# Kernel optimization log

Measured on AMD Instinct MI355X. Metric: run time of the kernel, lower is better.

Reference implementation:

```python
import jax, jax.numpy as jnp
import numpy as np

NUM_EMBEDDINGS = 8192
EMBEDDING_DIM = 256
COMMITMENT_COST = 0.25


def setup_inputs() -> dict:
    key = jax.random.key(0)
    k1, k2 = jax.random.split(key)
    inputs = jax.random.normal(k1, (16, 2048, EMBEDDING_DIM), dtype=jnp.float32)
    # codebook initialized uniform(-1/K, 1/K) as in the torch module
    codebook = jax.random.uniform(
        k2, (NUM_EMBEDDINGS, EMBEDDING_DIM), dtype=jnp.float32,
        minval=-1.0 / NUM_EMBEDDINGS, maxval=1.0 / NUM_EMBEDDINGS)
    return {"inputs": inputs, "codebook": codebook}


def reference(inputs, codebook):
    B, T, D = inputs.shape
    flat = inputs.reshape(-1, D)                      # [BT, D]
    distances = (
        jnp.sum(flat * flat, axis=1, keepdims=True)
        + jnp.sum(codebook * codebook, axis=1)
        - 2.0 * jnp.matmul(flat, codebook.T)
    )
    idx = jnp.argmin(distances, axis=1)               # [BT]
    quantized = codebook[idx].reshape(B, T, D)        # gather == one-hot @ codebook
    e_latent_loss = jnp.mean((jax.lax.stop_gradient(quantized) - inputs) ** 2)
    q_latent_loss = jnp.mean((quantized - jax.lax.stop_gradient(inputs)) ** 2)
    loss = q_latent_loss + COMMITMENT_COST * e_latent_loss
    # straight-through estimator
    quantized_st = inputs + jax.lax.stop_gradient(quantized - inputs)
    return quantized_st, idx.reshape(B, T), loss
```

## Files before the change

### kernel.cpp

```cpp
#include <hip/hip_runtime.h>
#include <hip/hip_bf16.h>
#include <stdint.h>

#define D      256
#define K      8192
#define NROWS  32768
#define QELEMS 8388608

typedef __attribute__((ext_vector_type(8))) short bf16x8;
typedef __attribute__((ext_vector_type(4))) float f32x4;
typedef unsigned int u32;
typedef unsigned short u16;

__device__ __forceinline__ u16 f2bf(float f) {
    u32 b = __float_as_uint(f);
    return (u16)((b + 0x7fffu + ((b >> 16) & 1u)) >> 16);
}

__global__ __launch_bounds__(256) void vq_prep_kernel(
    const float* __restrict__ cb, u16* __restrict__ ch,
    float* __restrict__ se, float* __restrict__ loss_sum) {
    int row = blockIdx.x * 4 + (threadIdx.x >> 6);
    int l = threadIdx.x & 63;
    float4 v = *(const float4*)(cb + (size_t)row * D + l * 4);
    ushort4 o;
    o.x = f2bf(v.x); o.y = f2bf(v.y); o.z = f2bf(v.z); o.w = f2bf(v.w);
    *(ushort4*)(ch + (size_t)row * D + l * 4) = o;
    float s = v.x * v.x + v.y * v.y + v.z * v.z + v.w * v.w;
    #pragma unroll
    for (int off = 32; off > 0; off >>= 1) s += __shfl_down(s, off, 64);
    if (l == 0) se[row] = s;
    if (blockIdx.x == 0 && threadIdx.x == 0) *loss_sum = 0.f;
}

__global__ __launch_bounds__(256) void vq_filter_kernel(
    const u16* __restrict__ ch, const float* __restrict__ x,
    const float* __restrict__ se, u32* __restrict__ cand)
{
    __shared__ u16 As[2][16384];

    const int tid  = threadIdx.x;
    const int lane = tid & 63;
    const int wave = tid >> 6;
    const int m_w  = wave & 1;
    const int n_w  = wave >> 1;
    const int l15  = lane & 15;
    const int l4   = lane >> 4;
    const int row0 = blockIdx.x * 64;

    bf16x8 Bf[2][8];
    #pragma unroll
    for (int nt = 0; nt < 2; ++nt) {
        const float* xr = x + (size_t)(row0 + n_w * 32 + nt * 16 + l15) * D + l4 * 8;
        #pragma unroll
        for (int c = 0; c < 8; ++c) {
            float4 a = *(const float4*)(xr + c * 32);
            float4 b = *(const float4*)(xr + c * 32 + 4);
            bf16x8 f;
            f[0] = (short)f2bf(a.x); f[1] = (short)f2bf(a.y);
            f[2] = (short)f2bf(a.z); f[3] = (short)f2bf(a.w);
            f[4] = (short)f2bf(b.x); f[5] = (short)f2bf(b.y);
            f[6] = (short)f2bf(b.z); f[7] = (short)f2bf(b.w);
            Bf[nt][c] = f;
        }
    }

    float b0[2], b1[2]; int c0[2], c1[2];
    #pragma unroll
    for (int nt = 0; nt < 2; ++nt) { b0[nt] = 1e30f; b1[nt] = 1e30f; c0[nt] = 0; c1[nt] = 0; }

    #pragma unroll
    for (int i = 0; i < 8; ++i) {
        int g = wave * 8 + i;
        const u16* gp = ch + (size_t)((g & 3) * 16 + l15) * D + (g >> 2) * 32 + l4 * 8;
        u16* lb = &As[0][(size_t)g * 512];
        __builtin_amdgcn_global_load_lds(
            (const __attribute__((address_space(1))) u32*)gp,
            (__attribute__((address_space(3))) u32*)lb, 16, 0, 0);
    }
    __syncthreads();

    int buf = 0;
    #pragma unroll 1
    for (int ct = 0; ct < 128; ++ct) {
        const int k0 = ct << 6;

        if (ct + 1 < 128) {
            const int kn = (ct + 1) << 6;
            #pragma unroll
            for (int i = 0; i < 8; ++i) {
                int g = wave * 8 + i;
                const u16* gp = ch + (size_t)(kn + (g & 3) * 16 + l15) * D + (g >> 2) * 32 + l4 * 8;
                u16* lb = &As[buf ^ 1][(size_t)g * 512];
                __builtin_amdgcn_global_load_lds(
                    (const __attribute__((address_space(1))) u32*)gp,
                    (__attribute__((address_space(3))) u32*)lb, 16, 0, 0);
            }
        }

        const u16* cb_t = &As[buf][0];
        f32x4 acc[2][2];
        #pragma unroll
        for (int mt = 0; mt < 2; ++mt)
            #pragma unroll
            for (int nt = 0; nt < 2; ++nt) acc[mt][nt] = (f32x4){0.f, 0.f, 0.f, 0.f};

        #pragma unroll
        for (int c = 0; c < 8; ++c) {
            bf16x8 Af0 = *(const bf16x8*)(cb_t + (size_t)((c * 4 + m_w * 2 + 0) * 64 + lane) * 8);
            bf16x8 Af1 = *(const bf16x8*)(cb_t + (size_t)((c * 4 + m_w * 2 + 1) * 64 + lane) * 8);
            acc[0][0] = __builtin_amdgcn_mfma_f32_16x16x32_bf16(Af0, Bf[0][c], acc[0][0], 0, 0, 0);
            acc[0][1] = __builtin_amdgcn_mfma_f32_16x16x32_bf16(Af0, Bf[1][c], acc[0][1], 0, 0, 0);
            acc[1][0] = __builtin_amdgcn_mfma_f32_16x16x32_bf16(Af1, Bf[0][c], acc[1][0], 0, 0, 0);
            acc[1][1] = __builtin_amdgcn_mfma_f32_16x16x32_bf16(Af1, Bf[1][c], acc[1][1], 0, 0, 0);
        }

        f32x4 sev[2];
        #pragma unroll
        for (int mt = 0; mt < 2; ++mt)
            sev[mt] = *(const f32x4*)(se + k0 + (m_w * 2 + mt) * 16 + l4 * 4);

        #pragma unroll
        for (int nt = 0; nt < 2; ++nt) {
            float tmn = 1e30f;
            #pragma unroll
            for (int mt = 0; mt < 2; ++mt)
                #pragma unroll
                for (int r = 0; r < 4; ++r)
                    tmn = fminf(tmn, fmaf(-2.f, acc[mt][nt][r], sev[mt][r]));
            if (tmn < b1[nt]) {
                #pragma unroll
                for (int mt = 0; mt < 2; ++mt)
                    #pragma unroll
                    for (int r = 0; r < 4; ++r) {
                        float t = fmaf(-2.f, acc[mt][nt][r], sev[mt][r]);
                        int  cv = k0 + (m_w * 2 + mt) * 16 + l4 * 4 + r;
                        bool in0 = t < b0[nt];
                        bool in1 = t < b1[nt];
                        float ob0 = b0[nt]; int oc0 = c0[nt];
                        b1[nt] = in0 ? ob0 : (in1 ? t  : b1[nt]);
                        c1[nt] = in0 ? oc0 : (in1 ? cv : c1[nt]);
                        b0[nt] = in0 ? t  : ob0;
                        c0[nt] = in0 ? cv : oc0;
                    }
            }
        }

        __syncthreads();
        buf ^= 1;
    }

    #pragma unroll
    for (int nt = 0; nt < 2; ++nt) {
        int row = row0 + n_w * 32 + nt * 16 + l15;
        int sl  = (m_w * 4 + l4) * 2;
        cand[(size_t)row * 16 + sl]     = (u32)c0[nt];
        cand[(size_t)row * 16 + sl + 1] = (u32)c1[nt];
    }
}

__global__ __launch_bounds__(1024) void vq_rescore_kernel(
    const float* __restrict__ x, const float* __restrict__ cb,
    const float* __restrict__ se, const u32* __restrict__ cand,
    float* __restrict__ out, float* __restrict__ loss_sum)
{
    const int wave = threadIdx.x >> 6;
    const int lane = threadIdx.x & 63;
    const int row  = blockIdx.x * 16 + wave;

    float4 xv = *(const float4*)(x + (size_t)row * D + lane * 4);
    float sx = xv.x * xv.x + xv.y * xv.y + xv.z * xv.z + xv.w * xv.w;
    #pragma unroll
    for (int o = 1; o < 64; o <<= 1) sx += __shfl_xor(sx, o, 64);

    u32 myc = cand[(size_t)row * 16 + (lane & 15)];
    float best = 1e30f; int bk = 0x7fffffff;
    #pragma unroll 4
    for (int j = 0; j < 16; ++j) {
        int code = __shfl((int)myc, j, 64);
        float4 ev = *(const float4*)(cb + (size_t)code * D + lane * 4);
        float p = xv.x * ev.x + xv.y * ev.y + xv.z * ev.z + xv.w * ev.w;
        #pragma unroll
        for (int o = 1; o < 64; o <<= 1) p += __shfl_xor(p, o, 64);
        float dist = (sx + se[code]) - 2.0f * p;
        if (dist < best || (dist == best && code < bk)) { best = dist; bk = code; }
    }

    float4 q = *(const float4*)(cb + (size_t)bk * D + lane * 4);
    *(float4*)(out + (size_t)row * D + lane * 4) = q;
    float dx = q.x - xv.x, dy = q.y - xv.y, dz = q.z - xv.z, dw = q.w - xv.w;
    float s = dx * dx + dy * dy + dz * dz + dw * dw;
    #pragma unroll
    for (int o = 1; o < 64; o <<= 1) s += __shfl_xor(s, o, 64);
    if (lane == 0) out[QELEMS + row] = (float)bk;

    __shared__ float red[16];
    if (lane == 0) red[wave] = s;
    __syncthreads();
    if (threadIdx.x == 0) {
        float t = 0.f;
        #pragma unroll
        for (int w2 = 0; w2 < 16; ++w2) t += red[w2];
        atomicAdd(loss_sum, t);
    }
}

__global__ void vq_fin_kernel(const float* __restrict__ loss_sum, float* __restrict__ out) {
    out[QELEMS + NROWS] = 1.25f * (*loss_sum) * (1.0f / (float)QELEMS);
}

extern "C" void kernel_launch(void* const* d_in, const int* in_sizes, int n_in,
                              void* d_out, int out_size, void* d_ws, size_t ws_size,
                              hipStream_t stream) {
    const float* x  = (const float*)d_in[0];
    const float* cb = (const float*)d_in[1];
    float* out = (float*)d_out;

    u16* ch = (u16*)d_out;

    char* ws = (char*)d_ws;
    float* loss_sum = (float*)ws;
    float* sebuf    = (float*)(ws + 4096);
    u32*   cand     = (u32*)(ws + 65536);

    vq_prep_kernel<<<K / 4, 256, 0, stream>>>(cb, ch, sebuf, loss_sum);
    vq_filter_kernel<<<NROWS / 64, 256, 0, stream>>>(ch, x, sebuf, cand);
    vq_rescore_kernel<<<NROWS / 16, 1024, 0, stream>>>(x, cb, sebuf, cand, out, loss_sum);
    vq_fin_kernel<<<1, 1, 0, stream>>>(loss_sum, out);
}
```

Measured before the change: 393.9 us.

## Give each wave all 64 rows and one codebook slice, merge top-2 via LDS

The filter kernel's wave tiling changes so each wave holds bf16 fragments for all 64 input rows and takes a single 16-code slice of every codebook tile. Each LDS A-fragment read now feeds four MFMAs instead of two, halving LDS traffic per MFMA, and only one se vector is loaded per tile. Per-lane top-2 lists are merged pairwise through shared memory at the end so the candidate count stays at 16 per row. The cost is more registers for the input fragments and a launch_bounds occupancy hint of 2, which can force spills or limit occupancy.

```diff
diff --git a/kernel.cpp b/kernel.cpp
--- a/kernel.cpp
+++ b/kernel.cpp
@@ -33,25 +33,23 @@
     if (blockIdx.x == 0 && threadIdx.x == 0) *loss_sum = 0.f;
 }
 
-__global__ __launch_bounds__(256) void vq_filter_kernel(
+__global__ __launch_bounds__(256, 2) void vq_filter_kernel(
     const u16* __restrict__ ch, const float* __restrict__ x,
     const float* __restrict__ se, u32* __restrict__ cand)
 {
-    __shared__ u16 As[2][16384];
+    __shared__ __align__(16) u16 As[2][16384];
 
     const int tid  = threadIdx.x;
     const int lane = tid & 63;
     const int wave = tid >> 6;
-    const int m_w  = wave & 1;
-    const int n_w  = wave >> 1;
     const int l15  = lane & 15;
     const int l4   = lane >> 4;
     const int row0 = blockIdx.x * 64;
 
-    bf16x8 Bf[2][8];
-    #pragma unroll
-    for (int nt = 0; nt < 2; ++nt) {
-        const float* xr = x + (size_t)(row0 + n_w * 32 + nt * 16 + l15) * D + l4 * 8;
+    bf16x8 Bf[4][8];
+    #pragma unroll
+    for (int nt = 0; nt < 4; ++nt) {
+        const float* xr = x + (size_t)(row0 + nt * 16 + l15) * D + l4 * 8;
         #pragma unroll
         for (int c = 0; c < 8; ++c) {
             float4 a = *(const float4*)(xr + c * 32);
@@ -65,9 +63,9 @@
         }
     }
 
-    float b0[2], b1[2]; int c0[2], c1[2];
-    #pragma unroll
-    for (int nt = 0; nt < 2; ++nt) { b0[nt] = 1e30f; b1[nt] = 1e30f; c0[nt] = 0; c1[nt] = 0; }
+    float b0[4], b1[4]; int c0[4], c1[4];
+    #pragma unroll
+    for (int nt = 0; nt < 4; ++nt) { b0[nt] = 1e30f; b1[nt] = 1e30f; c0[nt] = 0; c1[nt] = 0; }
 
     #pragma unroll
     for (int i = 0; i < 8; ++i) {
@@ -99,50 +97,41 @@
         }
 
         const u16* cb_t = &As[buf][0];
-        f32x4 acc[2][2];
-        #pragma unroll
-        for (int mt = 0; mt < 2; ++mt)
-            #pragma unroll
-            for (int nt = 0; nt < 2; ++nt) acc[mt][nt] = (f32x4){0.f, 0.f, 0.f, 0.f};
+        f32x4 acc[4];
+        #pragma unroll
+        for (int nt = 0; nt < 4; ++nt) acc[nt] = (f32x4){0.f, 0.f, 0.f, 0.f};
 
         #pragma unroll
         for (int c = 0; c < 8; ++c) {
-            bf16x8 Af0 = *(const bf16x8*)(cb_t + (size_t)((c * 4 + m_w * 2 + 0) * 64 + lane) * 8);
-            bf16x8 Af1 = *(const bf16x8*)(cb_t + (size_t)((c * 4 + m_w * 2 + 1) * 64 + lane) * 8);
-            acc[0][0] = __builtin_amdgcn_mfma_f32_16x16x32_bf16(Af0, Bf[0][c], acc[0][0], 0, 0, 0);
-            acc[0][1] = __builtin_amdgcn_mfma_f32_16x16x32_bf16(Af0, Bf[1][c], acc[0][1], 0, 0, 0);
-            acc[1][0] = __builtin_amdgcn_mfma_f32_16x16x32_bf16(Af1, Bf[0][c], acc[1][0], 0, 0, 0);
-            acc[1][1] = __builtin_amdgcn_mfma_f32_16x16x32_bf16(Af1, Bf[1][c], acc[1][1], 0, 0, 0);
-        }
-
-        f32x4 sev[2];
-        #pragma unroll
-        for (int mt = 0; mt < 2; ++mt)
-            sev[mt] = *(const f32x4*)(se + k0 + (m_w * 2 + mt) * 16 + l4 * 4);
-
-        #pragma unroll
-        for (int nt = 0; nt < 2; ++nt) {
-            float tmn = 1e30f;
-            #pragma unroll
-            for (int mt = 0; mt < 2; ++mt)
-                #pragma unroll
-                for (int r = 0; r < 4; ++r)
-                    tmn = fminf(tmn, fmaf(-2.f, acc[mt][nt][r], sev[mt][r]));
+            bf16x8 Af = *(const bf16x8*)(cb_t + (size_t)((c * 4 + wave) * 64 + lane) * 8);
+            acc[0] = __builtin_amdgcn_mfma_f32_16x16x32_bf16(Af, Bf[0][c], acc[0], 0, 0, 0);
+            acc[1] = __builtin_amdgcn_mfma_f32_16x16x32_bf16(Af, Bf[1][c], acc[1], 0, 0, 0);
+            acc[2] = __builtin_amdgcn_mfma_f32_16x16x32_bf16(Af, Bf[2][c], acc[2], 0, 0, 0);
+            acc[3] = __builtin_amdgcn_mfma_f32_16x16x32_bf16(Af, Bf[3][c], acc[3], 0, 0, 0);
+        }
+
+        f32x4 sev = *(const f32x4*)(se + k0 + wave * 16 + l4 * 4);
+
+        #pragma unroll
+        for (int nt = 0; nt < 4; ++nt) {
+            float t0 = fmaf(-2.f, acc[nt][0], sev[0]);
+            float t1 = fmaf(-2.f, acc[nt][1], sev[1]);
+            float t2 = fmaf(-2.f, acc[nt][2], sev[2]);
+            float t3 = fmaf(-2.f, acc[nt][3], sev[3]);
+            float tmn = fminf(fminf(t0, t1), fminf(t2, t3));
             if (tmn < b1[nt]) {
                 #pragma unroll
-                for (int mt = 0; mt < 2; ++mt)
-                    #pragma unroll
-                    for (int r = 0; r < 4; ++r) {
-                        float t = fmaf(-2.f, acc[mt][nt][r], sev[mt][r]);
-                        int  cv = k0 + (m_w * 2 + mt) * 16 + l4 * 4 + r;
-                        bool in0 = t < b0[nt];
-                        bool in1 = t < b1[nt];
-                        float ob0 = b0[nt]; int oc0 = c0[nt];
-                        b1[nt] = in0 ? ob0 : (in1 ? t  : b1[nt]);
-                        c1[nt] = in0 ? oc0 : (in1 ? cv : c1[nt]);
-                        b0[nt] = in0 ? t  : ob0;
-                        c0[nt] = in0 ? cv : oc0;
-                    }
+                for (int r = 0; r < 4; ++r) {
+                    float t = fmaf(-2.f, acc[nt][r], sev[r]);
+                    int  cv = k0 + wave * 16 + l4 * 4 + r;
+                    bool in0 = t < b0[nt];
+                    bool in1 = t < b1[nt];
+                    float ob0 = b0[nt]; int oc0 = c0[nt];
+                    b1[nt] = in0 ? ob0 : (in1 ? t  : b1[nt]);
+                    c1[nt] = in0 ? oc0 : (in1 ? cv : c1[nt]);
+                    b0[nt] = in0 ? t  : ob0;
+                    c0[nt] = in0 ? cv : oc0;
+                }
             }
         }
 
@@ -150,12 +139,32 @@
         buf ^= 1;
     }
 
-    #pragma unroll
-    for (int nt = 0; nt < 2; ++nt) {
-        int row = row0 + n_w * 32 + nt * 16 + l15;
-        int sl  = (m_w * 4 + l4) * 2;
-        cand[(size_t)row * 16 + sl]     = (u32)c0[nt];
-        cand[(size_t)row * 16 + sl + 1] = (u32)c1[nt];
+    float* Mv = (float*)&As[0][0];
+    u32*   Mc = (u32*)(Mv + 64 * 33);
+    #pragma unroll
+    for (int nt = 0; nt < 4; ++nt) {
+        int rl = nt * 16 + l15;
+        int g  = wave * 4 + l4;
+        Mv[rl * 33 + g * 2]     = b0[nt];
+        Mv[rl * 33 + g * 2 + 1] = b1[nt];
+        Mc[rl * 33 + g * 2]     = (u32)c0[nt];
+        Mc[rl * 33 + g * 2 + 1] = (u32)c1[nt];
+    }
+    __syncthreads();
+
+    for (int tsk = tid; tsk < 512; tsk += 256) {
+        int row = tsk >> 3, m = tsk & 7;
+        const float* v  = Mv + row * 33 + m * 4;
+        const u32*   cc = Mc + row * 33 + m * 4;
+        float v00 = v[0],  v01 = v[1],  v10 = v[2],  v11 = v[3];
+        u32   c00 = cc[0], c01 = cc[1], c10 = cc[2], c11 = cc[3];
+        bool  aw  = v00 <= v10;
+        u32   w0c = aw ? c00 : c10;
+        float s1  = aw ? v10 : v00; u32 s1c = aw ? c10 : c00;
+        float s2  = aw ? v01 : v11; u32 s2c = aw ? c01 : c11;
+        u32   w1c = (s2 <= s1) ? s2c : s1c;
+        cand[(size_t)(row0 + row) * 16 + m * 2]     = w0c;
+        cand[(size_t)(row0 + row) * 16 + m * 2 + 1] = w1c;
     }
 }
 
```

Result: slower. 405.1 us (+2.9%).
